# Kernel tuning notes

Measured on AMD Instinct MI355X. Metric: run time of the kernel, lower is better.

## Reference

```python
import jax, jax.numpy as jnp
import numpy as np

PAD = float(-2**32 + 1)
NUM_HEADS = 16
LN_EPS = 1e-5


def _split_heads(x, h):
    # torch.cat(torch.chunk(x, h, dim=2), dim=0): head-major stacking
    B, T, D = x.shape
    d = D // h
    return x.reshape(B, T, h, d).transpose(2, 0, 1, 3).reshape(h * B, T, d)


def _merge_heads(x, h):
    # torch.cat(torch.chunk(x, h, dim=0), dim=2)
    hB, T, d = x.shape
    B = hB // h
    return x.reshape(h, B, T, d).transpose(1, 2, 0, 3).reshape(B, T, h * d)


def setup_inputs() -> dict:
    key = jax.random.key(0)
    ks = jax.random.split(key, 12)
    B, T, D = 2, 2048, 1024
    s = 1.0 / np.sqrt(D)
    return {
        "q": jax.random.normal(ks[0], (B, T, D), jnp.float32),
        "k": jax.random.normal(ks[1], (B, T, D), jnp.float32),
        "v": jax.random.normal(ks[2], (B, T, D), jnp.float32),
        "mask": jax.random.randint(ks[3], (B, T), 0, 2, jnp.int32),
        "causality": 0,
        "edge_fea": jnp.zeros((1,), jnp.float32),
        "wq": jax.random.normal(ks[4], (D, D), jnp.float32) * s,
        "bq": jax.random.normal(ks[5], (D,), jnp.float32) * 0.01,
        "wk": jax.random.normal(ks[6], (D, D), jnp.float32) * s,
        "bk": jax.random.normal(ks[7], (D,), jnp.float32) * 0.01,
        "wv": jax.random.normal(ks[8], (D, D), jnp.float32) * s,
        "bv": jax.random.normal(ks[9], (D,), jnp.float32) * 0.01,
        "gamma": jnp.ones((D,), jnp.float32),
        "beta": jnp.zeros((D,), jnp.float32),
    }


def reference(q, k, v, mask, causality, edge_fea, wq, bq, wk, bk, wv, bv, gamma, beta):
    h = NUM_HEADS
    B, T, D = q.shape
    depth = D // h

    qh = _split_heads(q @ wq.T + bq, h)   # (h*B, T, depth)
    kh = _split_heads(k @ wk.T + bk, h)
    vh = _split_heads(v @ wv.T + bv, h)

    scores = jnp.einsum('ntd,nsd->nts', qh, kh) / jnp.sqrt(jnp.asarray(depth, qh.dtype))
    # key mask: repeat_interleave over dim 0 (batch-major), 1 => masked
    km = jnp.repeat(mask.astype(scores.dtype), h, axis=0)[:, None, :]  # (h*B,1,T)
    scores = scores + km * PAD
    if causality:
        tril = jnp.tril(jnp.ones((T, T), scores.dtype))
        scores = jnp.where(tril[None] == 0, jnp.full_like(scores, PAD), scores)
    attn = jax.nn.softmax(scores, axis=-1)
    ctx = jnp.einsum('nts,nsd->ntd', attn, vh)

    out = _merge_heads(ctx, h) + q  # dropout is identity in eval mode
    # LayerNorm over last dim
    mu = jnp.mean(out, axis=-1, keepdims=True)
    var = jnp.var(out, axis=-1, keepdims=True)
    out = (out - mu) / jnp.sqrt(var + LN_EPS) * gamma + beta
    return out
```

## Files before the change

### kernel.cpp

```cpp
#include <hip/hip_runtime.h>
#include <hip/hip_bf16.h>
#include <stdint.h>

#define B_ 2
#define T_ 2048
#define D_ 1024
#define H_ 16
#define DEPTH 64

typedef unsigned short u16;
typedef unsigned int u32;
typedef short bf16x8 __attribute__((ext_vector_type(8)));
typedef short bf16x4 __attribute__((ext_vector_type(4)));
typedef float f32x4 __attribute__((ext_vector_type(4)));
typedef float f32x16 __attribute__((ext_vector_type(16)));

#define MFMA16(a, b, c) __builtin_amdgcn_mfma_f32_16x16x32_bf16(a, b, c, 0, 0, 0)
#define MFMA32(a, b, c) __builtin_amdgcn_mfma_f32_32x32x16_bf16(a, b, c, 0, 0, 0)

#if __has_builtin(__builtin_amdgcn_exp2f)
#define EXP2(x) __builtin_amdgcn_exp2f(x)
#else
#define EXP2(x) __expf((x) * 0.6931471805599453f)
#endif

#define GLOAD_LDS(g, l)                                                      \
    __builtin_amdgcn_global_load_lds(                                        \
        (__attribute__((address_space(1))) void*)(g),                        \
        (__attribute__((address_space(3))) void*)(l), 16, 0, 0)

__device__ __forceinline__ float bf2f(u32 u) {
    union { u32 i; float f; } x; x.i = u << 16; return x.f;
}
__device__ __forceinline__ u16 f2bf(float f) {
    union { float f; u32 i; } x; x.f = f;
    u32 r = x.i + 0x7fffu + ((x.i >> 16) & 1u);
    return (u16)(r >> 16);
}
__device__ __forceinline__ uint2 pk4(float4 f) {
    return make_uint2((u32)f2bf(f.x) | ((u32)f2bf(f.y) << 16),
                      (u32)f2bf(f.z) | ((u32)f2bf(f.w) << 16));
}
__device__ __forceinline__ u32 cvtpk(float lo, float hi) {
    u32 r;
    asm("v_cvt_pk_bf16_f32 %0, %1, %2" : "=v"(r) : "v"(lo), "v"(hi));
    return r;
}
__device__ __forceinline__ bf16x8 pk_frag(u32 a, u32 b, u32 c, u32 d) {
    union { u32 u[4]; bf16x8 v; } x;
    x.u[0] = a; x.u[1] = b; x.u[2] = c; x.u[3] = d;
    return x.v;
}
__device__ __forceinline__ bf16x8 cat44(bf16x4 a, bf16x4 b) {
    bf16x8 r;
    r[0] = a[0]; r[1] = a[1]; r[2] = a[2]; r[3] = a[3];
    r[4] = b[0]; r[5] = b[1]; r[6] = b[2]; r[7] = b[3];
    return r;
}
__device__ __forceinline__ f32x16 zero16() {
    f32x16 z;
    #pragma unroll
    for (int i = 0; i < 16; ++i) z[i] = 0.f;
    return z;
}

__global__ __launch_bounds__(256) void conv_kernel(
    const float* __restrict__ s0, const float* __restrict__ s1, const float* __restrict__ s2,
    const float* __restrict__ s3, const float* __restrict__ s4, const float* __restrict__ s5,
    u16* __restrict__ xbf, u16* __restrict__ wbf)
{
    const int z = blockIdx.y;
    const float* src = (z == 0) ? s0 : (z == 1) ? s1 : (z == 2) ? s2
                     : (z == 3) ? s3 : (z == 4) ? s4 : s5;
    u16* dst = (z < 3) ? (xbf + (size_t)z * 4194304) : (wbf + (size_t)(z - 3) * 1048576);
    const size_t nel = (z < 3) ? 4194304u : 1048576u;
    for (size_t i = ((size_t)blockIdx.x * 256 + threadIdx.x) * 8; i < nel;
         i += (size_t)gridDim.x * 2048) {
        float4 a = *(const float4*)(src + i);
        float4 b = *(const float4*)(src + i + 4);
        uint2 lo = pk4(a), hi = pk4(b);
        *(uint4*)(dst + i) = make_uint4(lo.x, lo.y, hi.x, hi.y);
    }
}

__global__ __launch_bounds__(256, 3) void proj_mfma(
    const u16* __restrict__ xbf, const u16* __restrict__ wbf,
    const float* __restrict__ bq, const float* __restrict__ bk, const float* __restrict__ bv,
    u16* __restrict__ qh, u16* __restrict__ kh, u16* __restrict__ vt)
{
    __shared__ __attribute__((aligned(16))) u16 As[128 * 64];
    __shared__ __attribute__((aligned(16))) u16 Bs[128 * 64];

    const int z = blockIdx.z;
    const u16* A = xbf + (size_t)z * 4194304;
    const u16* W = wbf + (size_t)z * 1048576;
    const float* bias = (z == 0) ? bq : (z == 1) ? bk : bv;

    const int tid = threadIdx.x, w = tid >> 6, lane = tid & 63;
    const int quad = lane >> 4, l16 = lane & 15;
    const int m0 = blockIdx.y * 128, n0 = blockIdx.x * 128;
    const int wm = (w & 1) * 64, wn = (w >> 1) * 64;
    const int srow = lane >> 3;
    const int schunk = (lane & 7) ^ srow;

    f32x4 acc[4][4];
    #pragma unroll
    for (int mi = 0; mi < 4; ++mi)
        #pragma unroll
        for (int ni = 0; ni < 4; ++ni) acc[mi][ni] = (f32x4){0.f, 0.f, 0.f, 0.f};

    const size_t ar = (size_t)(m0 + 32 * w + srow);
    const size_t br = (size_t)(n0 + 32 * w + srow);

    for (int k0 = 0; k0 < D_; k0 += 64) {
        __syncthreads();
        #pragma unroll
        for (int i = 0; i < 4; ++i) {
            GLOAD_LDS(A + (ar + 8 * i) * D_ + k0 + schunk * 8, &As[(32 * w + 8 * i) * 64]);
            GLOAD_LDS(W + (br + 8 * i) * D_ + k0 + schunk * 8, &Bs[(32 * w + 8 * i) * 64]);
        }
        __syncthreads();

        #pragma unroll
        for (int kg = 0; kg < 2; ++kg) {
            const int ch = ((4 * kg + quad) ^ (l16 & 7)) * 8;
            bf16x8 af[4], bf[4];
            #pragma unroll
            for (int mi = 0; mi < 4; ++mi)
                af[mi] = *(const bf16x8*)&As[(wm + 16 * mi + l16) * 64 + ch];
            #pragma unroll
            for (int ni = 0; ni < 4; ++ni)
                bf[ni] = *(const bf16x8*)&Bs[(wn + 16 * ni + l16) * 64 + ch];
            #pragma unroll
            for (int mi = 0; mi < 4; ++mi)
                #pragma unroll
                for (int ni = 0; ni < 4; ++ni)
                    acc[mi][ni] = MFMA16(af[mi], bf[ni], acc[mi][ni]);
        }
    }

    float bl[4];
    #pragma unroll
    for (int ni = 0; ni < 4; ++ni) bl[ni] = bias[n0 + wn + ni * 16 + l16];

    #pragma unroll
    for (int mi = 0; mi < 4; ++mi) {
        const int mb = m0 + wm + mi * 16 + quad * 4;
        #pragma unroll
        for (int ni = 0; ni < 4; ++ni) {
            const int nn = n0 + wn + ni * 16 + l16;
            const int head = nn >> 6, d = nn & 63;
            if (z < 2) {
                u16* outp = (z == 0) ? qh : kh;
                #pragma unroll
                for (int r = 0; r < 4; ++r) {
                    const int m = mb + r;
                    const int b = m >> 11, t = m & (T_ - 1);
                    outp[((size_t)(head * B_ + b) * T_ + t) * DEPTH + d] =
                        f2bf(acc[mi][ni][r] + bl[ni]);
                }
            } else {
                const int b = mb >> 11, t = mb & (T_ - 1);
                float4 f = make_float4(acc[mi][ni][0] + bl[ni], acc[mi][ni][1] + bl[ni],
                                       acc[mi][ni][2] + bl[ni], acc[mi][ni][3] + bl[ni]);
                *(uint2*)(vt + ((size_t)(head * B_ + b) * DEPTH + d) * T_ + t) = pk4(f);
            }
        }
    }
}

__global__ __launch_bounds__(256, 4) void attn_kernel(
    const u16* __restrict__ qh, const u16* __restrict__ kh, const u16* __restrict__ vt,
    const int* __restrict__ maskp, const int* __restrict__ causp,
    u16* __restrict__ po, float* __restrict__ pl)
{
    __shared__ __attribute__((aligned(16))) u16 Ks[2][64 * 64];
    __shared__ __attribute__((aligned(16))) u16 Vs[2][64 * 64];
    __shared__ __attribute__((aligned(16))) float padf[1024];

    const int n  = blockIdx.y;
    const int qt = blockIdx.x;
    const int kk = blockIdx.z;
    const int kbase = kk * 1024;
    const int head = n >> 1, bi = n & 1;
    const int mrow = n >> 4;
    const int caus = causp[0];

    const int tid  = threadIdx.x;
    const int w    = tid >> 6, lane = tid & 63;
    const int l32  = lane & 31, h = lane >> 5;
    const size_t base  = (size_t)n * T_ * DEPTH;
    const size_t vbase = (size_t)n * DEPTH * T_;
    const size_t elems = (size_t)B_ * T_ * D_;

    const float C1  = 0.18033688011112042f;
    const float PL2 = -6.2e9f;

    {
        const int i0 = tid * 4;
        int4 m = *(const int4*)(maskp + (size_t)mrow * T_ + kbase + i0);
        padf[i0 + 0] = (float)m.x * PL2; padf[i0 + 1] = (float)m.y * PL2;
        padf[i0 + 2] = (float)m.z * PL2; padf[i0 + 3] = (float)m.w * PL2;
    }

    const int qg = qt * 128 + w * 32 + l32;
    bf16x8 aq[4];
    #pragma unroll
    for (int c = 0; c < 4; ++c)
        aq[c] = *(const bf16x8*)(qh + base + (size_t)qg * DEPTH + c * 16 + h * 8);

    f32x16 O0 = zero16(), O1 = zero16();
    float lp = 0.f;

    const int g_row = w * 16 + (lane >> 3);
    const int g_ch  = (lane & 7) ^ ((lane >> 3) & 7);
    const u16* ksrc = kh + base + (size_t)g_row * DEPTH + g_ch * 8;
    const u16* vsrc = vt + vbase + (size_t)g_row * T_ + g_ch * 8;

#define STAGE(bf_, t0_)                                                           \
    do {                                                                          \
        GLOAD_LDS(ksrc + (size_t)(t0_) * DEPTH,       &Ks[bf_][(w * 16) * 64]);   \
        GLOAD_LDS(ksrc + (size_t)((t0_) + 8) * DEPTH, &Ks[bf_][(w * 16 + 8) * 64]); \
        GLOAD_LDS(vsrc + (t0_),                       &Vs[bf_][(w * 16) * 64]);   \
        GLOAD_LDS(vsrc + (size_t)8 * T_ + (t0_),      &Vs[bf_][(w * 16 + 8) * 64]); \
    } while (0)

    STAGE(0, kbase);
    __syncthreads();

    for (int it = 0; it < 16; ++it) {
        const int cur = it & 1;
        if (it < 15) STAGE(cur ^ 1, kbase + (it + 1) * 64);

        const int lt0 = it * 64;
        bf16x8 pa[2][2];
        #pragma unroll
        for (int kb = 0; kb < 2; ++kb) {
            const int krow = kb * 32 + l32;
            const u16* krp = &Ks[cur][krow * 64];
            const int ksw = krow & 7;
            f32x16 st = zero16();
            #pragma unroll
            for (int c = 0; c < 4; ++c) {
                bf16x8 kf = *(const bf16x8*)(krp + (((c * 2 + h) ^ ksw) * 8));
                st = MFMA32(kf, aq[c], st);
            }
            u32 pk[8];
            #pragma unroll
            for (int g = 0; g < 4; ++g) {
                f32x4 pv = *(const f32x4*)&padf[lt0 + kb * 32 + g * 8 + h * 4];
                #pragma unroll
                for (int m2 = 0; m2 < 2; ++m2) {
                    const int r0 = g * 4 + m2 * 2;
                    float v0 = fmaf(st[r0],     C1, pv[m2 * 2]);
                    float v1 = fmaf(st[r0 + 1], C1, pv[m2 * 2 + 1]);
                    if (caus) {
                        const int kg = kbase + lt0 + kb * 32 + g * 8 + h * 4 + m2 * 2;
                        if (kg     > qg) v0 = PL2;
                        if (kg + 1 > qg) v1 = PL2;
                    }
                    const float e0 = EXP2(v0), e1 = EXP2(v1);
                    lp += e0 + e1;
                    pk[g * 2 + m2] = cvtpk(e0, e1);
                }
            }
            pa[kb][0] = pk_frag(pk[0], pk[1], pk[2], pk[3]);
            pa[kb][1] = pk_frag(pk[4], pk[5], pk[6], pk[7]);
        }

        #pragma unroll
        for (int dblk = 0; dblk < 2; ++dblk) {
            const int d = dblk * 32 + l32;
            const u16* vrp = &Vs[cur][d * 64 + 4 * h];
            const int vsw = d & 7;
            #pragma unroll
            for (int kb = 0; kb < 2; ++kb)
                #pragma unroll
                for (int kc = 0; kc < 2; ++kc) {
                    const int p0 = (kb * 4 + kc * 2) ^ vsw;
                    bf16x4 vlo = *(const bf16x4*)(vrp + p0 * 8);
                    bf16x4 vhi = *(const bf16x4*)(vrp + (p0 ^ 1) * 8);
                    bf16x8 vf = cat44(vlo, vhi);
                    if (dblk == 0) O0 = MFMA32(pa[kb][kc], vf, O0);
                    else           O1 = MFMA32(pa[kb][kc], vf, O1);
                }
        }
        __syncthreads();
    }
#undef STAGE

    lp += __shfl_xor(lp, 32, 64);
    u16* pop = po + (size_t)kk * elems;
    float* plp = pl + (size_t)kk * 32 * T_;
    if (lane < 32)
        plp[(size_t)n * T_ + qt * 128 + w * 32 + l32] = lp;

    #pragma unroll
    for (int r = 0; r < 16; ++r) {
        const int q = qt * 128 + w * 32 + (r & 3) + 8 * (r >> 2) + 4 * h;
        const size_t rb = ((size_t)bi * T_ + q) * D_ + head * DEPTH + l32;
        pop[rb]      = f2bf(O0[r]);
        pop[rb + 32] = f2bf(O1[r]);
    }
}

__global__ __launch_bounds__(256) void fuse_ln(
    const u16* __restrict__ po, const float* __restrict__ pl,
    const float* __restrict__ qin,
    const float* __restrict__ gamma, const float* __restrict__ beta,
    float* __restrict__ out)
{
    const int row = blockIdx.x;
    const int bi = row >> 11, t = row & (T_ - 1);
    const int tid = threadIdx.x;
    const size_t elems = (size_t)B_ * T_ * D_;

    const int head = tid >> 4;
    const size_t li = (size_t)(head * B_ + bi) * T_ + t;
    const float l = pl[li] + pl[32 * T_ + li];
    const float inv = 1.0f / fmaxf(l, 1e-30f);

    const size_t basei = (size_t)row * D_ + (tid << 2);
    uint2 a = *(const uint2*)(po + basei);
    uint2 b = *(const uint2*)(po + elems + basei);
    float4 qv = *(const float4*)(qin + basei);
    float x[4];
    x[0] = (bf2f(a.x & 0xffffu) + bf2f(b.x & 0xffffu)) * inv + qv.x;
    x[1] = (bf2f(a.x >> 16)     + bf2f(b.x >> 16))     * inv + qv.y;
    x[2] = (bf2f(a.y & 0xffffu) + bf2f(b.y & 0xffffu)) * inv + qv.z;
    x[3] = (bf2f(a.y >> 16)     + bf2f(b.y >> 16))     * inv + qv.w;

    float s  = x[0] + x[1] + x[2] + x[3];
    float s2 = x[0]*x[0] + x[1]*x[1] + x[2]*x[2] + x[3]*x[3];
    #pragma unroll
    for (int off = 1; off < 64; off <<= 1) {
        s  += __shfl_xor(s, off, 64);
        s2 += __shfl_xor(s2, off, 64);
    }
    __shared__ float rs[4], rs2[4];
    const int wid = tid >> 6;
    if ((tid & 63) == 0) { rs[wid] = s; rs2[wid] = s2; }
    __syncthreads();
    s  = rs[0] + rs[1] + rs[2] + rs[3];
    s2 = rs2[0] + rs2[1] + rs2[2] + rs2[3];
    const float mean = s * (1.0f / (float)D_);
    const float var  = s2 * (1.0f / (float)D_) - mean * mean;
    const float rstd = rsqrtf(var + 1e-5f);
    float4 g = *(const float4*)(gamma + (tid << 2));
    float4 bb = *(const float4*)(beta + (tid << 2));
    float4 r;
    r.x = (x[0] - mean) * rstd * g.x + bb.x;
    r.y = (x[1] - mean) * rstd * g.y + bb.y;
    r.z = (x[2] - mean) * rstd * g.z + bb.z;
    r.w = (x[3] - mean) * rstd * g.w + bb.w;
    *(float4*)(out + basei) = r;
}

extern "C" void kernel_launch(void* const* d_in, const int* in_sizes, int n_in,
                              void* d_out, int out_size, void* d_ws, size_t ws_size,
                              hipStream_t stream)
{
    (void)in_sizes; (void)n_in; (void)out_size; (void)ws_size;
    const float* q    = (const float*)d_in[0];
    const float* k    = (const float*)d_in[1];
    const float* v    = (const float*)d_in[2];
    const int* mask = (const int*)d_in[3];
    const int* caus = (const int*)d_in[4];
    const float* wq = (const float*)d_in[6];
    const float* bq = (const float*)d_in[7];
    const float* wk = (const float*)d_in[8];
    const float* bk = (const float*)d_in[9];
    const float* wv = (const float*)d_in[10];
    const float* bv = (const float*)d_in[11];
    const float* gamma = (const float*)d_in[12];
    const float* beta  = (const float*)d_in[13];
    float* out = (float*)d_out;

    const size_t elems = (size_t)B_ * T_ * D_;
    u16* qh  = (u16*)d_ws;
    u16* kh  = qh + elems;
    u16* vt  = kh + elems;
    u16* xbf = vt + elems;
    u16* wbf = xbf + 3 * elems;
    u16* po   = xbf;
    float* pl = (float*)(po + 2 * elems);

    conv_kernel<<<dim3(512, 6), 256, 0, stream>>>(q, k, v, wq, wk, wv, xbf, wbf);
    proj_mfma<<<dim3(8, 32, 3), 256, 0, stream>>>(xbf, wbf, bq, bk, bv, qh, kh, vt);

    dim3 agrid(T_ / 128, H_ * B_, 2);
    attn_kernel<<<agrid, 256, 0, stream>>>(qh, kh, vt, mask, caus, po, pl);

    fuse_ln<<<B_ * T_, 256, 0, stream>>>(po, pl, q, gamma, beta, out);
}
```

Before: 220.4 us.

## Permute V layout for 16-byte LDS reads, explicit vmcnt waits, and block swizzle

The V-projection epilogue now writes the transposed V with a bit permutation of t. The attention kernel can then load each MFMA B fragment with a single 16-byte LDS read instead of two 8-byte reads plus a concatenation. The compiler-inserted __syncthreads is replaced by explicit s_waitcnt vmcnt plus raw barriers, so the prefetch of the next K/V tile can stay in flight while the current tile is consumed. Block indices are also remapped so that consecutive workgroups spread across heads and splits, which is meant to improve cache locality. The risk is that the layout permutation must exactly match the fragment ordering, and the vmcnt counts must match the number of loads issued.

```diff
diff --git a/kernel.cpp b/kernel.cpp
--- a/kernel.cpp
+++ b/kernel.cpp
@@ -11,7 +11,6 @@
 typedef unsigned short u16;
 typedef unsigned int u32;
 typedef short bf16x8 __attribute__((ext_vector_type(8)));
-typedef short bf16x4 __attribute__((ext_vector_type(4)));
 typedef float f32x4 __attribute__((ext_vector_type(4)));
 typedef float f32x16 __attribute__((ext_vector_type(16)));
 
@@ -29,6 +28,14 @@
         (__attribute__((address_space(1))) void*)(g),                        \
         (__attribute__((address_space(3))) void*)(l), 16, 0, 0)
 
+#define WAITVM(n) asm volatile("s_waitcnt vmcnt(" #n ")" ::: "memory")
+#define BARRIER()                                                            \
+    do {                                                                     \
+        asm volatile("" ::: "memory");                                       \
+        __builtin_amdgcn_s_barrier();                                        \
+        asm volatile("" ::: "memory");                                       \
+    } while (0)
+
 __device__ __forceinline__ float bf2f(u32 u) {
     union { u32 i; float f; } x; x.i = u << 16; return x.f;
 }
@@ -50,12 +57,6 @@
     union { u32 u[4]; bf16x8 v; } x;
     x.u[0] = a; x.u[1] = b; x.u[2] = c; x.u[3] = d;
     return x.v;
-}
-__device__ __forceinline__ bf16x8 cat44(bf16x4 a, bf16x4 b) {
-    bf16x8 r;
-    r[0] = a[0]; r[1] = a[1]; r[2] = a[2]; r[3] = a[3];
-    r[4] = b[0]; r[5] = b[1]; r[6] = b[2]; r[7] = b[3];
-    return r;
 }
 __device__ __forceinline__ f32x16 zero16() {
     f32x16 z;
@@ -161,9 +162,10 @@
                 }
             } else {
                 const int b = mb >> 11, t = mb & (T_ - 1);
+                const int tp = (t & ~12) | ((t & 4) << 1) | ((t & 8) >> 1);
                 float4 f = make_float4(acc[mi][ni][0] + bl[ni], acc[mi][ni][1] + bl[ni],
                                        acc[mi][ni][2] + bl[ni], acc[mi][ni][3] + bl[ni]);
-                *(uint2*)(vt + ((size_t)(head * B_ + b) * DEPTH + d) * T_ + t) = pk4(f);
+                *(uint2*)(vt + ((size_t)(head * B_ + b) * DEPTH + d) * T_ + tp) = pk4(f);
             }
         }
     }
@@ -178,9 +180,12 @@
     __shared__ __attribute__((aligned(16))) u16 Vs[2][64 * 64];
     __shared__ __attribute__((aligned(16))) float padf[1024];
 
-    const int n  = blockIdx.y;
-    const int qt = blockIdx.x;
-    const int kk = blockIdx.z;
+    const int lin = blockIdx.x + 16 * blockIdx.y + 512 * blockIdx.z;
+    const int swz = (lin & 7) * 128 + (lin >> 3);
+    const int qt = swz & 15;
+    const int n  = (swz >> 4) & 31;
+    const int kk = swz >> 9;
+
     const int kbase = kk * 1024;
     const int head = n >> 1, bi = n & 1;
     const int mrow = n >> 4;
@@ -230,7 +235,13 @@
 
     for (int it = 0; it < 16; ++it) {
         const int cur = it & 1;
-        if (it < 15) STAGE(cur ^ 1, kbase + (it + 1) * 64);
+        if (it < 15) {
+            STAGE(cur ^ 1, kbase + (it + 1) * 64);
+            WAITVM(4);
+        } else {
+            WAITVM(0);
+        }
+        BARRIER();
 
         const int lt0 = it * 64;
         bf16x8 pa[2][2];
@@ -271,21 +282,19 @@
         #pragma unroll
         for (int dblk = 0; dblk < 2; ++dblk) {
             const int d = dblk * 32 + l32;
-            const u16* vrp = &Vs[cur][d * 64 + 4 * h];
+            const u16* vrp = &Vs[cur][d * 64];
             const int vsw = d & 7;
             #pragma unroll
             for (int kb = 0; kb < 2; ++kb)
                 #pragma unroll
                 for (int kc = 0; kc < 2; ++kc) {
-                    const int p0 = (kb * 4 + kc * 2) ^ vsw;
-                    bf16x4 vlo = *(const bf16x4*)(vrp + p0 * 8);
-                    bf16x4 vhi = *(const bf16x4*)(vrp + (p0 ^ 1) * 8);
-                    bf16x8 vf = cat44(vlo, vhi);
+                    const int ch = (kb * 4 + kc * 2 + h) ^ vsw;
+                    bf16x8 vf = *(const bf16x8*)(vrp + ch * 8);
                     if (dblk == 0) O0 = MFMA32(pa[kb][kc], vf, O0);
                     else           O1 = MFMA32(pa[kb][kc], vf, O1);
                 }
         }
-        __syncthreads();
+        BARRIER();
     }
 #undef STAGE
 
```

New measurement: 214.6 us. 2.6% less time.
